# Optimization experiments

Hardware: AMD Instinct MI355X
Metric: run time of the kernel (lower is better)

## Reference

```python
import jax, jax.numpy as jnp
import numpy as np

D = 1024            # BIGNET_DIM
GS = 16             # group_size
NG = D * D // GS    # groups per layer = 65536
N_LAYERS = 18       # 6 blocks * 3 linears
LORA_LAYERS = {0: 0, 6: 1, 12: 2}  # linear index -> lora slot (first linear of blocks 0,2,4)
RANK = 32
BATCH = 16384
EPS = 1e-5


def setup_inputs() -> dict:
    key = jax.random.key(0)
    ks = jax.random.split(key, 6)
    x = jax.random.normal(ks[0], (BATCH, D), dtype=jnp.float32)
    w_q = jax.random.randint(ks[1], (N_LAYERS, NG, GS), 0, 16, dtype=jnp.int32)
    w_norm = jax.random.uniform(ks[2], (N_LAYERS, NG, 1), dtype=jnp.float32)
    bias = jax.random.normal(ks[3], (N_LAYERS, D), dtype=jnp.float32) * 0.02
    lora_a = jax.random.normal(ks[4], (3, RANK, D), dtype=jnp.float32) * (1.0 / np.sqrt(D))
    lora_b = jax.random.normal(ks[5], (3, D, RANK), dtype=jnp.float32) * 0.02
    ln_w = jnp.ones((6, D), dtype=jnp.float32)
    ln_b = jnp.zeros((6, D), dtype=jnp.float32)
    return {"x": x, "w_q": w_q, "w_norm": w_norm, "bias": bias,
            "lora_a": lora_a, "lora_b": lora_b, "ln_w": ln_w, "ln_b": ln_b}


def _dequant(q, n):
    # block_dequantize_4bit: codes in [0,15] -> [-norm, +norm] per group
    return ((q.astype(jnp.float32) / 15.0) * 2.0 - 1.0) * n  # [NG, GS]


def reference(x, w_q, w_norm, bias, lora_a, lora_b, ln_w, ln_b):
    h = x
    for blk in range(6):
        for pos in range(3):
            l = blk * 3 + pos
            W = _dequant(w_q[l], w_norm[l]).reshape(D, D)  # [out, in]
            out = h @ W.T + bias[l]
            if l in LORA_LAYERS:
                i = LORA_LAYERS[l]
                out = out + (h @ lora_a[i].T) @ lora_b[i].T
            if pos < 2:
                out = jax.nn.relu(out)
            h = out
        mu = jnp.mean(h, axis=-1, keepdims=True)
        var = jnp.mean(jnp.square(h - mu), axis=-1, keepdims=True)
        h = (h - mu) * jax.lax.rsqrt(var + EPS) * ln_w[blk] + ln_b[blk]
    return h
```

## Files before the change

kernel.cpp:

```cpp
#include <hip/hip_runtime.h>
#include <cstdint>
#include <cstddef>


typedef short  bf16x8 __attribute__((ext_vector_type(8)));
typedef float  f32x4  __attribute__((ext_vector_type(4)));

__device__ __forceinline__ unsigned short f2bf(float f) {
  unsigned int u = __builtin_bit_cast(unsigned int, f);
  u += 0x7FFFu + ((u >> 16) & 1u);
  return (unsigned short)(u >> 16);
}

__device__ __forceinline__ void async_copy16(void* lds, const void* g) {
  __builtin_amdgcn_global_load_lds(
      (const __attribute__((address_space(1))) void*)(uintptr_t)(g),
      (__attribute__((address_space(3))) void*)(unsigned int)(uintptr_t)(lds),
      16, 0, 0);
}

__global__ __launch_bounds__(256) void dequant_kernel(
    const int* __restrict__ wq, const float* __restrict__ wn,
    const float* __restrict__ lora_a, const float* __restrict__ lora_b,
    unsigned short* __restrict__ Wbf) {
  const int l   = blockIdx.y;
  const int t   = threadIdx.x;
  const int blk = blockIdx.x;
  const long base = (long)l * 1048576;
  const float s = 2.0f / 15.0f;

  int4  q[4];
  float nrm[4];
#pragma unroll
  for (int k = 0; k < 4; ++k) {
    const int i4 = blk * 1024 + k * 256 + t;
    q[k]   = *(const int4*)(wq + base + (long)i4 * 4);
    nrm[k] = wn[l * 65536 + (i4 >> 2)];
  }

  float v[4][4];
#pragma unroll
  for (int k = 0; k < 4; ++k) {
    v[k][0] = ((float)q[k].x * s - 1.0f) * nrm[k];
    v[k][1] = ((float)q[k].y * s - 1.0f) * nrm[k];
    v[k][2] = ((float)q[k].z * s - 1.0f) * nrm[k];
    v[k][3] = ((float)q[k].w * s - 1.0f) * nrm[k];
  }

  const int slot = (l == 0) ? 0 : (l == 6) ? 1 : (l == 12) ? 2 : -1;
  if (slot >= 0) {
    const float* A = lora_a + slot * 32768 + t * 4;
    const float* B = lora_b + slot * 32768 + blk * 128;
#pragma unroll 8
    for (int r = 0; r < 32; ++r) {
      const float4 a4 = *(const float4*)(A + r * 1024);
#pragma unroll
      for (int k = 0; k < 4; ++k) {
        const float br = B[k * 32 + r];
        v[k][0] = fmaf(br, a4.x, v[k][0]);
        v[k][1] = fmaf(br, a4.y, v[k][1]);
        v[k][2] = fmaf(br, a4.z, v[k][2]);
        v[k][3] = fmaf(br, a4.w, v[k][3]);
      }
    }
  }

#pragma unroll
  for (int k = 0; k < 4; ++k) {
    unsigned short u[4] = {f2bf(v[k][0]), f2bf(v[k][1]),
                           f2bf(v[k][2]), f2bf(v[k][3])};
    const long e0 = base + ((long)blk * 1024 + k * 256 + t) * 4;
    *(uint2*)(Wbf + e0) = *(uint2*)u;
  }
}

__global__ __launch_bounds__(256) void cvt_bf16_kernel(
    const float* __restrict__ in, unsigned short* __restrict__ out) {
  const long b0 = (long)blockIdx.x * 4096 + threadIdx.x * 4;
  float4 v[4];
#pragma unroll
  for (int k = 0; k < 4; ++k) v[k] = *(const float4*)(in + b0 + k * 1024);
#pragma unroll
  for (int k = 0; k < 4; ++k) {
    unsigned short u[4] = {f2bf(v[k].x), f2bf(v[k].y), f2bf(v[k].z), f2bf(v[k].w)};
    *(ushort4*)(out + b0 + k * 1024) = *(ushort4*)u;
  }
}

template <int MODE>
__global__ __launch_bounds__(512, 2) void gemm8_kernel(
    const unsigned short* __restrict__ H,
    const unsigned short* __restrict__ W,
    const float* __restrict__ bias,
    unsigned short* __restrict__ outb,
    float* __restrict__ outf) {
  extern __shared__ char smem[];

  const int tid = threadIdx.x;
  const int w   = tid >> 6;
  const int ln  = tid & 63;
  const int wm  = w >> 2;
  const int wn  = w & 3;

  const int b  = blockIdx.x;
  const int s  = (b & 7) * 32 + (b >> 3);
  const int m0 = (s >> 2) * 256;
  const int n0 = (s & 3) * 256;

  const int gc    = (ln & 7) ^ ((ln >> 3) & 7);
  const int rowst = w * 8 + (ln >> 3);
  const unsigned eA = (unsigned)(m0 + rowst) * 1024u + gc * 8;
  const unsigned eB = (unsigned)(n0 + rowst) * 1024u + gc * 8;
  const int wofs = w * 1024;

  const int quad = ln >> 4;
  const int lrow = ln & 15;
  const int sw   = lrow & 7;
  const int c0   = ((quad)     ^ sw) * 16;
  const int c1   = ((quad + 4) ^ sw) * 16;
  const int aoff = (wm * 128 + lrow) * 128;
  const int boff = (wn * 64  + lrow) * 128;

#define STAGE_A(T_, D_, F_, J_)                                                \
  async_copy16(smem + (D_) * 65536 + (F_) * 16384 + (J_) * 8192 + wofs,        \
               H + eA + (unsigned)((T_) * 64 + ((F_) * 128 + (J_) * 64) * 1024))
#define STAGE_B(T_, D_, F_, J_)                                                \
  async_copy16(smem + (D_) * 65536 + 32768 + (F_) * 16384 + (J_) * 8192 + wofs,\
               W + eB + (unsigned)((T_) * 64 + ((F_) * 128 + (J_) * 64) * 1024))
#define MM16(AV, BV, I0, J0)                                                   \
  {                                                                            \
    _Pragma("unroll") for (int i_ = 0; i_ < 4; ++i_) {                         \
      _Pragma("unroll") for (int j_ = 0; j_ < 2; ++j_) {                       \
        acc[(I0) + i_][(J0) + j_] = __builtin_amdgcn_mfma_f32_16x16x32_bf16(   \
            AV[i_][0], BV[j_][0], acc[(I0) + i_][(J0) + j_], 0, 0, 0);         \
        acc[(I0) + i_][(J0) + j_] = __builtin_amdgcn_mfma_f32_16x16x32_bf16(   \
            AV[i_][1], BV[j_][1], acc[(I0) + i_][(J0) + j_], 0, 0, 0);         \
      }                                                                        \
    }                                                                          \
  }
#define LDSUB4(DST, BASE, OFF)                                                 \
  {                                                                            \
    _Pragma("unroll") for (int i_ = 0; i_ < 4; ++i_) {                         \
      DST[i_][0] = *(const bf16x8*)((BASE) + (OFF) + i_ * 2048 + c0);          \
      DST[i_][1] = *(const bf16x8*)((BASE) + (OFF) + i_ * 2048 + c1);          \
    }                                                                          \
  }
#define LDSUB2(DST, BASE, OFF)                                                 \
  {                                                                            \
    _Pragma("unroll") for (int j_ = 0; j_ < 2; ++j_) {                         \
      DST[j_][0] = *(const bf16x8*)((BASE) + (OFF) + j_ * 2048 + c0);          \
      DST[j_][1] = *(const bf16x8*)((BASE) + (OFF) + j_ * 2048 + c1);          \
    }                                                                          \
  }

  f32x4 acc[8][4];
#pragma unroll
  for (int i = 0; i < 8; ++i)
#pragma unroll
    for (int j = 0; j < 4; ++j) acc[i][j] = (f32x4){0.f, 0.f, 0.f, 0.f};

  STAGE_A(0, 0, 0, 0); STAGE_A(0, 0, 0, 1);
  STAGE_A(0, 0, 1, 0); STAGE_A(0, 0, 1, 1);
  STAGE_B(0, 0, 0, 0); STAGE_B(0, 0, 0, 1);
  STAGE_B(0, 0, 1, 0); STAGE_B(0, 0, 1, 1);
  asm volatile("" ::: "memory");
  STAGE_A(1, 1, 0, 0); STAGE_A(1, 1, 0, 1);
  STAGE_A(1, 1, 1, 0); STAGE_A(1, 1, 1, 1);
  asm volatile("s_waitcnt vmcnt(4)" ::: "memory");
  __builtin_amdgcn_s_barrier();

  bf16x8 a0[4][2], a1[4][2], bb[2][2];

#pragma unroll 2
  for (int kt = 0; kt < 16; ++kt) {
    const int BUF = kt & 1;
    const char* At = smem + BUF * 65536;
    const char* Bt = At + 32768;
    const int  nb = BUF ^ 1;
    const bool ib = (kt < 15);
    const bool ia = (kt < 14);

    LDSUB4(a0, At, aoff);
    LDSUB2(bb, Bt, boff);
    if (ib) { STAGE_B(kt + 1, nb, 0, 0); STAGE_B(kt + 1, nb, 0, 1); }
    __builtin_amdgcn_s_barrier();
    asm volatile("s_waitcnt lgkmcnt(0)" ::: "memory");
    __builtin_amdgcn_s_setprio(1);
    MM16(a0, bb, 0, 0);
    __builtin_amdgcn_s_setprio(0);
    __builtin_amdgcn_s_barrier();

    LDSUB4(a1, At, aoff + 8192);
    if (ib) { STAGE_B(kt + 1, nb, 1, 0); STAGE_B(kt + 1, nb, 1, 1); }
    __builtin_amdgcn_s_barrier();
    asm volatile("s_waitcnt lgkmcnt(0)" ::: "memory");
    __builtin_amdgcn_s_setprio(1);
    MM16(a1, bb, 4, 0);
    __builtin_amdgcn_s_setprio(0);
    __builtin_amdgcn_s_barrier();

    LDSUB2(bb, Bt, boff + 4096);
    if (ia) { STAGE_A(kt + 2, BUF, 0, 0); STAGE_A(kt + 2, BUF, 0, 1); }
    __builtin_amdgcn_s_barrier();
    asm volatile("s_waitcnt lgkmcnt(0)" ::: "memory");
    __builtin_amdgcn_s_setprio(1);
    MM16(a1, bb, 4, 2);
    __builtin_amdgcn_s_setprio(0);
    __builtin_amdgcn_s_barrier();

    if (ia) { STAGE_A(kt + 2, BUF, 1, 0); STAGE_A(kt + 2, BUF, 1, 1); }
    __builtin_amdgcn_s_barrier();
    __builtin_amdgcn_s_setprio(1);
    MM16(a0, bb, 0, 2);
    __builtin_amdgcn_s_setprio(0);
    if (kt < 14) {
      asm volatile("s_waitcnt vmcnt(4)" ::: "memory");
    } else if (kt == 14) {
      asm volatile("s_waitcnt vmcnt(0)" ::: "memory");
    }
    __builtin_amdgcn_s_barrier();
  }

#undef LDSUB2
#undef LDSUB4
#undef MM16
#undef STAGE_B
#undef STAGE_A

#pragma unroll
  for (int nt = 0; nt < 4; ++nt) {
    const int n = n0 + wn * 64 + nt * 16 + lrow;
    const float bs = bias[n];
#pragma unroll
    for (int mt = 0; mt < 8; ++mt) {
      const int mb = m0 + wm * 128 + mt * 16 + quad * 4;
      const f32x4 v = acc[mt][nt];
#pragma unroll
      for (int r = 0; r < 4; ++r) {
        float o = v[r] + bs;
        if (MODE == 0) {
          o = fmaxf(o, 0.0f);
          outb[(size_t)(mb + r) * 1024 + n] = f2bf(o);
        } else {
          outf[(size_t)(mb + r) * 1024 + n] = o;
        }
      }
    }
  }
}

__global__ __launch_bounds__(256) void ln_kernel(
    const float* __restrict__ in, const float* __restrict__ lnw,
    const float* __restrict__ lnb, unsigned short* __restrict__ outb,
    float* __restrict__ outf, int wf32) {
  const int wv = threadIdx.x >> 6;
  const int ln = threadIdx.x & 63;
  const int row = blockIdx.x * 4 + wv;
  const float* p = in + (size_t)row * 1024;

  float4 v[4];
  float s = 0.f, q = 0.f;
#pragma unroll
  for (int c = 0; c < 4; ++c) {
    v[c] = *(const float4*)(p + c * 256 + ln * 4);
    s += v[c].x + v[c].y + v[c].z + v[c].w;
    q += v[c].x * v[c].x + v[c].y * v[c].y + v[c].z * v[c].z + v[c].w * v[c].w;
  }
#pragma unroll
  for (int off = 32; off; off >>= 1) {
    s += __shfl_xor(s, off);
    q += __shfl_xor(q, off);
  }
  const float mu  = s * (1.0f / 1024.0f);
  const float var = q * (1.0f / 1024.0f) - mu * mu;
  const float rs  = rsqrtf(var + 1e-5f);

#pragma unroll
  for (int c = 0; c < 4; ++c) {
    const int col = c * 256 + ln * 4;
    const float4 w4 = *(const float4*)(lnw + col);
    const float4 b4 = *(const float4*)(lnb + col);
    const float y0 = (v[c].x - mu) * rs * w4.x + b4.x;
    const float y1 = (v[c].y - mu) * rs * w4.y + b4.y;
    const float y2 = (v[c].z - mu) * rs * w4.z + b4.z;
    const float y3 = (v[c].w - mu) * rs * w4.w + b4.w;
    unsigned short u[4] = {f2bf(y0), f2bf(y1), f2bf(y2), f2bf(y3)};
    *(ushort4*)(outb + (size_t)row * 1024 + col) = *(ushort4*)u;
    if (wf32) {
      float4 y = make_float4(y0, y1, y2, y3);
      *(float4*)(outf + (size_t)row * 1024 + col) = y;
    }
  }
}

extern "C" void kernel_launch(void* const* d_in, const int* in_sizes, int n_in,
                              void* d_out, int out_size, void* d_ws, size_t ws_size,
                              hipStream_t stream) {
  const float* x    = (const float*)d_in[0];
  const int*   wq   = (const int*)d_in[1];
  const float* wn   = (const float*)d_in[2];
  const float* bias = (const float*)d_in[3];
  const float* la   = (const float*)d_in[4];
  const float* lb   = (const float*)d_in[5];
  const float* lnw  = (const float*)d_in[6];
  const float* lnb  = (const float*)d_in[7];
  float* out = (float*)d_out;

  char* ws = (char*)d_ws;
  unsigned short* Wbf = (unsigned short*)ws;
  unsigned short* hA  = (unsigned short*)(ws + 37748736);
  unsigned short* hB  = (unsigned short*)(ws + 37748736 + 33554432);

  dequant_kernel<<<dim3(256, 18), 256, 0, stream>>>(wq, wn, la, lb, Wbf);
  cvt_bf16_kernel<<<4096, 256, 0, stream>>>(x, hA);

  for (int blk = 0; blk < 6; ++blk) {
    const int l = blk * 3;
    gemm8_kernel<0><<<256, 512, 131072, stream>>>(
        hA, Wbf + (size_t)l * 1048576, bias + l * 1024, hB, nullptr);
    gemm8_kernel<0><<<256, 512, 131072, stream>>>(
        hB, Wbf + (size_t)(l + 1) * 1048576, bias + (l + 1) * 1024, hA, nullptr);
    gemm8_kernel<1><<<256, 512, 131072, stream>>>(
        hA, Wbf + (size_t)(l + 2) * 1048576, bias + (l + 2) * 1024, nullptr, out);
    ln_kernel<<<4096, 256, 0, stream>>>(
        out, lnw + blk * 1024, lnb + blk * 1024, hA, out, blk == 5 ? 1 : 0);
  }
}
```

Before: 985.0 us.

## Prefetch next-tile LDS fragments across iterations and reorder B staging layout

Restructures the GEMM main loop so the A and B register fragments for the next k-tile are read from LDS during the current iteration. This removes the explicit lgkmcnt(0) waits before each MFMA group and reorders the quadrant MFMA sequence to match. It also changes how B and A tiles are split across waves for async global-to-LDS staging, so the first B half a wave needs arrives earlier. Finer vmcnt waits are added to keep correctness. The risks are more register pressure and reliance on compiler-inserted waits for LDS reads.

```diff
diff --git a/kernel.cpp b/kernel.cpp
--- a/kernel.cpp
+++ b/kernel.cpp
@@ -107,11 +107,12 @@
   const int m0 = (s >> 2) * 256;
   const int n0 = (s & 3) * 256;
 
-  const int gc    = (ln & 7) ^ ((ln >> 3) & 7);
-  const int rowst = w * 8 + (ln >> 3);
-  const unsigned eA = (unsigned)(m0 + rowst) * 1024u + gc * 8;
-  const unsigned eB = (unsigned)(n0 + rowst) * 1024u + gc * 8;
-  const int wofs = w * 1024;
+  const int gc = (ln & 7) ^ ((ln >> 3) & 7);
+  const unsigned eA2 = (unsigned)(m0 + w * 8 + (ln >> 3)) * 1024u + gc * 8;
+  const int wofsA = w * 1024;
+  const unsigned eB2 =
+      (unsigned)(n0 + (w >> 2) * 64 + (w & 3) * 8 + (ln >> 3)) * 1024u + gc * 8;
+  const int wofsB = (w >> 2) * 8192 + (w & 3) * 1024;
 
   const int quad = ln >> 4;
   const int lrow = ln & 15;
@@ -122,11 +123,12 @@
   const int boff = (wn * 64  + lrow) * 128;
 
 #define STAGE_A(T_, D_, F_, J_)                                                \
-  async_copy16(smem + (D_) * 65536 + (F_) * 16384 + (J_) * 8192 + wofs,        \
-               H + eA + (unsigned)((T_) * 64 + ((F_) * 128 + (J_) * 64) * 1024))
+  async_copy16(smem + (D_) * 65536 + (J_) * 16384 + (F_) * 8192 + wofsA,       \
+               H + eA2 + (unsigned)((T_) * 64 + ((J_) * 128 + (F_) * 64) * 1024))
 #define STAGE_B(T_, D_, F_, J_)                                                \
-  async_copy16(smem + (D_) * 65536 + 32768 + (F_) * 16384 + (J_) * 8192 + wofs,\
-               W + eB + (unsigned)((T_) * 64 + ((F_) * 128 + (J_) * 64) * 1024))
+  async_copy16(smem + (D_) * 65536 + 32768 + (J_) * 16384 + (F_) * 4096 + wofsB,\
+               W + eB2 + (unsigned)((T_) * 64 + ((J_) * 128 + (F_) * 32) * 1024))
+#define VMCNT(N_) asm volatile("s_waitcnt vmcnt(" #N_ ")" ::: "memory")
 #define MM16(AV, BV, I0, J0)                                                   \
   {                                                                            \
     _Pragma("unroll") for (int i_ = 0; i_ < 4; ++i_) {                         \
@@ -166,64 +168,65 @@
   asm volatile("" ::: "memory");
   STAGE_A(1, 1, 0, 0); STAGE_A(1, 1, 0, 1);
   STAGE_A(1, 1, 1, 0); STAGE_A(1, 1, 1, 1);
-  asm volatile("s_waitcnt vmcnt(4)" ::: "memory");
+  VMCNT(4);
   __builtin_amdgcn_s_barrier();
 
-  bf16x8 a0[4][2], a1[4][2], bb[2][2];
-
-#pragma unroll 2
+  bf16x8 aX[4][2], aY[4][2], b0f[2][2], b1f[2][2];
+  LDSUB4(aX, smem, aoff);
+  LDSUB2(b0f, smem + 32768, boff);
+
   for (int kt = 0; kt < 16; ++kt) {
     const int BUF = kt & 1;
+    const int nb  = BUF ^ 1;
     const char* At = smem + BUF * 65536;
+    const char* Ao = smem + nb  * 65536;
     const char* Bt = At + 32768;
-    const int  nb = BUF ^ 1;
+    const char* Bo = Ao + 32768;
     const bool ib = (kt < 15);
     const bool ia = (kt < 14);
 
-    LDSUB4(a0, At, aoff);
-    LDSUB2(bb, Bt, boff);
+    LDSUB2(b1f, Bt, boff + 4096);
     if (ib) { STAGE_B(kt + 1, nb, 0, 0); STAGE_B(kt + 1, nb, 0, 1); }
     __builtin_amdgcn_s_barrier();
-    asm volatile("s_waitcnt lgkmcnt(0)" ::: "memory");
     __builtin_amdgcn_s_setprio(1);
-    MM16(a0, bb, 0, 0);
+    MM16(aX, b0f, 0, 0);
     __builtin_amdgcn_s_setprio(0);
     __builtin_amdgcn_s_barrier();
 
-    LDSUB4(a1, At, aoff + 8192);
+    LDSUB4(aY, At, aoff + 8192);
     if (ib) { STAGE_B(kt + 1, nb, 1, 0); STAGE_B(kt + 1, nb, 1, 1); }
-    __builtin_amdgcn_s_barrier();
-    asm volatile("s_waitcnt lgkmcnt(0)" ::: "memory");
+    if (ib) VMCNT(6);
+    __builtin_amdgcn_s_barrier();
     __builtin_amdgcn_s_setprio(1);
-    MM16(a1, bb, 4, 0);
+    MM16(aX, b1f, 0, 2);
     __builtin_amdgcn_s_setprio(0);
     __builtin_amdgcn_s_barrier();
 
-    LDSUB2(bb, Bt, boff + 4096);
+    if (ib) LDSUB4(aX, Ao, aoff);
     if (ia) { STAGE_A(kt + 2, BUF, 0, 0); STAGE_A(kt + 2, BUF, 0, 1); }
-    __builtin_amdgcn_s_barrier();
-    asm volatile("s_waitcnt lgkmcnt(0)" ::: "memory");
+    if (ia) { VMCNT(4); }
+    else if (kt == 14) { VMCNT(2); }
+    __builtin_amdgcn_s_barrier();
     __builtin_amdgcn_s_setprio(1);
-    MM16(a1, bb, 4, 2);
+    MM16(aY, b1f, 4, 2);
     __builtin_amdgcn_s_setprio(0);
     __builtin_amdgcn_s_barrier();
 
     if (ia) { STAGE_A(kt + 2, BUF, 1, 0); STAGE_A(kt + 2, BUF, 1, 1); }
     __builtin_amdgcn_s_barrier();
     __builtin_amdgcn_s_setprio(1);
-    MM16(a0, bb, 0, 2);
+    MM16(aY, b0f, 4, 0);
     __builtin_amdgcn_s_setprio(0);
-    if (kt < 14) {
-      asm volatile("s_waitcnt vmcnt(4)" ::: "memory");
-    } else if (kt == 14) {
-      asm volatile("s_waitcnt vmcnt(0)" ::: "memory");
-    }
+    if (ib) LDSUB2(b0f, Bo, boff);
+    if (ia) { VMCNT(4); }
+    else if (kt == 14) { VMCNT(0); }
     __builtin_amdgcn_s_barrier();
   }
 
 #undef LDSUB2
 #undef LDSUB4
 #undef MM16
+#undef VMCNT
 #undef STAGE_B
 #undef STAGE_A
 
```

Measured after the change: 1.039 ms. 5.4% more time.
